# Optimization experiments

Measured on AMD Instinct MI355X. Metric: run time of the kernel, lower is better.

## Reference

```python
import jax, jax.numpy as jnp
import numpy as np

B, L, D, H = 32, 512, 512, 8          # batch(=num_nodes), seq len, model_size, num_heads
HD = D // H                            # head size
E_DIM, N_EDGES, N_PATHS = 128, 4096, 1024  # edge_dim (hardcoded 128), edge table, #(src,dst) pairs
MAXD = H                               # max_path_distance == num_heads


def setup_inputs() -> dict:
    rng = jax.random.key(0)
    ks = jax.random.split(rng, 16)
    n = lambda k, s: jax.random.normal(k, s, jnp.float32)
    idx = jnp.arange(N_PATHS)
    inp = {
        'query': n(ks[0], (B, L, D)),
        'key':   n(ks[1], (B, L, D)),
        'value': n(ks[2], (B, L, D)),
        'mask':  jnp.ones((B, 1, 1, L), jnp.float32),
        'edge_attr': n(ks[3], (N_EDGES, E_DIM)),
        'path_src': (idx // B).astype(jnp.int32),   # all (src,dst) node pairs
        'path_dst': (idx % B).astype(jnp.int32),
        'path_edges': jax.random.randint(ks[4], (N_PATHS, MAXD), 0, N_EDGES),
        'path_lens': jax.random.randint(ks[5], (N_PATHS,), 1, MAXD + 1),
        # learned params
        'WQ': n(ks[6], (D, D)) * 0.02, 'bQ': jnp.zeros((D,), jnp.float32),
        'WK': n(ks[7], (D, D)) * 0.02, 'bK': jnp.zeros((D,), jnp.float32),
        'WV': n(ks[8], (D, D)) * 0.02, 'bV': jnp.zeros((D,), jnp.float32),
        'WO': n(ks[9], (D, D)) * 0.02, 'bO': jnp.zeros((D,), jnp.float32),
        'edge_vector': n(ks[10], (MAXD, E_DIM)) * 0.05,  # EdgeEncoding weight
        'b_vec': n(ks[11], (MAXD,)) * 0.05,              # SpatialEncoding weight
        'b_scale': jnp.float32(0.001),
        'c_scale': jnp.float32(0.001),
    }
    return inp


def reference(query, key, value, mask, edge_attr, path_src, path_dst, path_edges,
              path_lens, WQ, bQ, WK, bK, WV, bV, WO, bO, edge_vector, b_vec,
              b_scale, c_scale):
    def split_heads(x):  # [B,L,D] -> [B,H,L,HD]
        return x.reshape(B, L, H, HD).transpose(0, 2, 1, 3)

    q = split_heads(jnp.einsum('bld,de->ble', query, WQ) + bQ)
    k = split_heads(jnp.einsum('bld,de->ble', key, WK) + bK)
    v = split_heads(jnp.einsum('bld,de->ble', value, WV) + bV)

    score = jnp.einsum('bhqd,bhkd->bhqk', q, k) / jnp.sqrt(jnp.float32(HD))

    pl = jnp.minimum(path_lens, MAXD).astype(jnp.int32)  # clipped path lengths

    # SpatialEncoding: spatial[src,dst] = b_vec[min(len,maxd)-1]
    spatial = jnp.zeros((B, B), jnp.float32).at[path_src, path_dst].set(b_vec[pl - 1])
    b_mean = spatial.mean(axis=1)  # [B]

    # EdgeEncoding: cij[src,dst] = mean_k <edge_vector[k], edge_attr[path[k]]>
    pe = edge_attr[path_edges]                       # [P,MAXD,E]  batched gather
    dots = jnp.einsum('ke,pke->pk', edge_vector, pe)  # [P,MAXD]
    kmask = (jnp.arange(MAXD)[None, :] < pl[:, None]).astype(jnp.float32)
    cvals = jnp.where(pl > 0, (dots * kmask).sum(1) / jnp.maximum(pl, 1), 0.0)
    cij = jnp.zeros((B, B), jnp.float32).at[path_src, path_dst].set(cvals)
    c_mean = cij.mean(axis=1)  # [B]

    bias = (b_scale * b_mean + c_scale * c_mean)[:, None, None, None]
    score = score + bias + (1.0 - mask) * (-1e9)

    alpha = jax.nn.softmax(score, axis=-1)
    ctx = jnp.einsum('bhqk,bhkd->bhqd', alpha, v)
    ctx = ctx.transpose(0, 2, 1, 3).reshape(B, L, D)
    return jnp.einsum('bld,de->ble', ctx, WO) + bO
```

## Files before the change

kernel.cpp:

```cpp
#include <hip/hip_runtime.h>
#include <hip/hip_bf16.h>

#define B_  32
#define L_  512
#define D_  512
#define H_  8
#define HD_ 64

typedef __attribute__((ext_vector_type(8))) short bf16x8;
typedef __attribute__((ext_vector_type(4))) short bf16x4;
typedef __attribute__((ext_vector_type(4))) float f32x4;

__device__ __forceinline__ short f2bf(float f) {
  union { float f; unsigned u; } x; x.f = f;
  unsigned r = x.u + 0x7FFFu + ((x.u >> 16) & 1u);
  return (short)(r >> 16);
}

__device__ __forceinline__ void gll16(const void* g, void* l) {
  __builtin_amdgcn_global_load_lds(
      (const __attribute__((address_space(1))) unsigned int*)g,
      (__attribute__((address_space(3))) unsigned int*)l, 16, 0, 0);
}

__device__ __forceinline__ bf16x8 cvt8(f32x4 a, f32x4 b) {
  union { __hip_bfloat162 h[4]; bf16x8 v; } u;
  u.h[0] = __float22bfloat162_rn(float2{a[0], a[1]});
  u.h[1] = __float22bfloat162_rn(float2{a[2], a[3]});
  u.h[2] = __float22bfloat162_rn(float2{b[0], b[1]});
  u.h[3] = __float22bfloat162_rn(float2{b[2], b[3]});
  return u.v;
}

#define DS_FENCE() do { asm volatile("s_waitcnt lgkmcnt(0)" ::: "memory"); \
                        __builtin_amdgcn_sched_barrier(0); } while (0)

__global__ __launch_bounds__(256) void wt_kernel(
    const float* __restrict__ WQ, const float* __restrict__ WK,
    const float* __restrict__ WV, const float* __restrict__ WO,
    short* __restrict__ wt) {
  __shared__ float tile[32][33];
  int wz = blockIdx.z;
  const float* W = (wz == 0) ? WQ : (wz == 1) ? WK : (wz == 2) ? WV : WO;
  int k0 = blockIdx.y * 32, n0 = blockIdx.x * 32;
  int tr = threadIdx.x >> 5, tc = threadIdx.x & 31;
#pragma unroll
  for (int i = 0; i < 4; ++i)
    tile[tr + i * 8][tc] = W[(size_t)(k0 + tr + i * 8) * D_ + n0 + tc];
  __syncthreads();
#pragma unroll
  for (int i = 0; i < 4; ++i)
    wt[((size_t)wz * D_ + n0 + tr + i * 8) * D_ + k0 + tc] =
        f2bf(tile[tc][tr + i * 8]);
}

__global__ __launch_bounds__(256, 3) void gemm_qkv(
    const float* __restrict__ Xq, const float* __restrict__ Xk,
    const float* __restrict__ Xv, const short* __restrict__ wt,
    const float* __restrict__ bQ, const float* __restrict__ bK,
    const float* __restrict__ bV,
    short* __restrict__ q_ws, short* __restrict__ k_ws,
    short* __restrict__ vt_ws) {
  __shared__ __align__(16) char lds[49152];

  int mode = blockIdx.z;
  const float* A = (mode == 0) ? Xq : (mode == 1) ? Xk : Xv;
  const short* WT = wt + (size_t)mode * D_ * D_;
  const float* bias = (mode == 0) ? bQ : (mode == 1) ? bK : bV;

  int wgid = blockIdx.x + 4 * blockIdx.y;
  int rr_ = wgid >> 3;
  int m0 = ((wgid & 7) * 16 + (rr_ >> 2)) * 128;
  int n0 = (rr_ & 3) * 128;

  int tid = threadIdx.x, lane = tid & 63, w = tid >> 6;
  int wr = w >> 1, wc = w & 1, g = lane >> 4, lr = lane & 15;

  int qa = lane >> 3, ca = (lane & 7) ^ qa;
  int qb = lane >> 2, cb = (lane & 3) ^ ((lane >> 3) & 3);

  auto stage = [&](int ks, int bs) {
    char* Ab = lds + bs * 16384;
    char* Bb = lds + 32768 + bs * 8192;
#pragma unroll
    for (int j = 0; j < 4; ++j) {
      int e = w * 4 + j, row = e * 8 + qa;
      gll16(A + (size_t)(m0 + row) * D_ + ks * 32 + ca * 4, Ab + e * 1024);
    }
#pragma unroll
    for (int j = 0; j < 2; ++j) {
      int e = w * 2 + j, row = e * 16 + qb;
      gll16(WT + (size_t)(n0 + row) * D_ + ks * 32 + cb * 8, Bb + e * 1024);
    }
  };

  stage(0, 0);
  __syncthreads();

  f32x4 acc[4][4] = {};
#pragma unroll
  for (int ks = 0; ks < 16; ++ks) {
    if (ks < 15) stage(ks + 1, (ks + 1) & 1);
    const char* Ab = lds + (ks & 1) * 16384;
    const char* Bb = lds + 32768 + (ks & 1) * 8192;
    bf16x8 af[4], bf_[4];
#pragma unroll
    for (int i = 0; i < 4; ++i) {
      int row = wr * 64 + i * 16 + lr;
      f32x4 lo = *(const f32x4*)(Ab + row * 128 + (((2 * g) ^ (lr & 7)) << 4));
      f32x4 hi = *(const f32x4*)(Ab + row * 128 + (((2 * g + 1) ^ (lr & 7)) << 4));
      af[i] = cvt8(lo, hi);
    }
#pragma unroll
    for (int i = 0; i < 4; ++i) {
      int row = wc * 64 + i * 16 + lr;
      bf_[i] = *(const bf16x8*)(Bb + row * 64 + ((g ^ ((lr >> 1) & 3)) << 4));
    }
#pragma unroll
    for (int mi = 0; mi < 4; ++mi)
#pragma unroll
      for (int nj = 0; nj < 4; ++nj)
        acc[mi][nj] = __builtin_amdgcn_mfma_f32_16x16x32_bf16(
            af[mi], bf_[nj], acc[mi][nj], 0, 0, 0);
    __syncthreads();
  }

#pragma unroll
  for (int mi = 0; mi < 4; ++mi) {
#pragma unroll
    for (int nj = 0; nj < 4; ++nj) {
      int n = n0 + wc * 64 + nj * 16 + lr;
      float bb = bias[n];
      int h = n >> 6, hd = n & 63;
#pragma unroll
      for (int rr = 0; rr < 4; ++rr) {
        int m = m0 + wr * 64 + mi * 16 + g * 4 + rr;
        int b = m >> 9, l = m & 511;
        short v = f2bf(acc[mi][nj][rr] + bb);
        if (mode == 0)
          q_ws[(((size_t)b * H_ + h) * L_ + l) * HD_ + hd] = v;
        else if (mode == 1)
          k_ws[(((size_t)b * H_ + h) * L_ + l) * HD_ + hd] = v;
        else
          vt_ws[(((size_t)b * H_ + h) * HD_ + hd) * L_ + l] = v;
      }
    }
  }
}

__global__ __launch_bounds__(256, 4) void attn_kernel(
    const short* __restrict__ q_ws, const short* __restrict__ k_ws,
    const short* __restrict__ vt_ws, const float* __restrict__ mask,
    short* __restrict__ ctx_ws) {
  __shared__ __align__(16) char lds[40960];
  int wg = blockIdx.x;
  int bh   = (wg & 7) * 32 + (wg >> 6);
  int qblk = (wg >> 3) & 7;
  int b = bh >> 3, h = bh & 7;
  int tid = threadIdx.x, lane = tid & 63, w = tid >> 6;
  int g = lane >> 4, lr = lane & 15;
  char* Pl = lds + 32768 + w * 2048;
  int qbase = qblk * 64 + w * 16;

  const short* Qh  = q_ws  + (size_t)bh * (L_ * HD_);
  const short* Kh  = k_ws  + (size_t)bh * (L_ * HD_);
  const short* VTh = vt_ws + (size_t)bh * (HD_ * L_);
  const float* mrow = mask + (size_t)b * L_;

  bf16x8 aq0 = *(const bf16x8*)(Qh + (size_t)(qbase + lr) * HD_ + g * 8);
  bf16x8 aq1 = *(const bf16x8*)(Qh + (size_t)(qbase + lr) * HD_ + 32 + g * 8);

  int rowin = lane >> 3;
  int sch8 = ((lane & 7) ^ rowin) * 8;

#pragma unroll
  for (int j = 0; j < 2; ++j) {
    int e = w * 2 + j, row = e * 8 + rowin;
    gll16(Kh + (size_t)row * HD_ + sch8, lds + e * 1024);
    gll16(VTh + (size_t)row * L_ + sch8, lds + 16384 + e * 1024);
  }
  __syncthreads();

  f32x4 c[4] = {};
  float m[4] = {-1e30f, -1e30f, -1e30f, -1e30f};
  float sum[4] = {0.f, 0.f, 0.f, 0.f};

  for (int ch = 0; ch < 8; ++ch) {
    const char* Kb = lds + (ch & 1) * 8192;
    const char* Vb = lds + 16384 + (ch & 1) * 8192;
    if (ch < 7) {
      char* Kn = lds + ((ch + 1) & 1) * 8192;
      char* Vn = lds + 16384 + ((ch + 1) & 1) * 8192;
#pragma unroll
      for (int j = 0; j < 2; ++j) {
        int e = w * 2 + j, row = e * 8 + rowin;
        gll16(Kh + ((size_t)(ch + 1) * 64 + row) * HD_ + sch8, Kn + e * 1024);
        gll16(VTh + (size_t)row * L_ + (ch + 1) * 64 + sch8, Vn + e * 1024);
      }
    }
    float mb[4];
#pragma unroll
    for (int kt = 0; kt < 4; ++kt)
      mb[kt] = (1.0f - mrow[ch * 64 + kt * 16 + lr]) * -1e9f;

    f32x4 s[4];
#pragma unroll
    for (int kt = 0; kt < 4; ++kt) {
      int row = kt * 16 + lr;
      bf16x8 bk0 = *(const bf16x8*)(Kb + row * 128 + ((g ^ (lr & 7)) << 4));
      bf16x8 bk1 = *(const bf16x8*)(Kb + row * 128 + (((4 + g) ^ (lr & 7)) << 4));
      f32x4 a = {0.f, 0.f, 0.f, 0.f};
      a = __builtin_amdgcn_mfma_f32_16x16x32_bf16(aq0, bk0, a, 0, 0, 0);
      a = __builtin_amdgcn_mfma_f32_16x16x32_bf16(aq1, bk1, a, 0, 0, 0);
#pragma unroll
      for (int rr = 0; rr < 4; ++rr) a[rr] = a[rr] * 0.125f + mb[kt];
      s[kt] = a;
    }

    float pmax[4], scl[4];
#pragma unroll
    for (int rr = 0; rr < 4; ++rr)
      pmax[rr] = fmaxf(fmaxf(s[0][rr], s[1][rr]), fmaxf(s[2][rr], s[3][rr]));
#pragma unroll
    for (int off = 1; off < 16; off <<= 1)
#pragma unroll
      for (int rr = 0; rr < 4; ++rr)
        pmax[rr] = fmaxf(pmax[rr], __shfl_xor(pmax[rr], off, 64));
#pragma unroll
    for (int rr = 0; rr < 4; ++rr) {
      float mn = fmaxf(m[rr], pmax[rr]);
      scl[rr] = __expf(m[rr] - mn);
      m[rr] = mn;
      sum[rr] *= scl[rr];
    }
#pragma unroll
    for (int nt = 0; nt < 4; ++nt)
#pragma unroll
      for (int rr = 0; rr < 4; ++rr) c[nt][rr] *= scl[rr];

#pragma unroll
    for (int kt = 0; kt < 4; ++kt) {
      int col2 = (kt * 16 + lr) * 2;
#pragma unroll
      for (int rr = 0; rr < 4; ++rr) {
        float p = __expf(s[kt][rr] - m[rr]);
        sum[rr] += p;
        int row = g * 4 + rr;
        *(short*)(Pl + row * 128 + (col2 ^ ((row & 7) << 4))) = f2bf(p);
      }
    }
    DS_FENCE();

#pragma unroll
    for (int kk = 0; kk < 2; ++kk) {
      bf16x8 ap = *(const bf16x8*)(Pl + lr * 128 +
                                   (((kk * 4 + g) ^ (lr & 7)) << 4));
#pragma unroll
      for (int nt = 0; nt < 4; ++nt) {
        int row = nt * 16 + lr;
        bf16x8 bv = *(const bf16x8*)(Vb + row * 128 +
                                     (((kk * 4 + g) ^ (lr & 7)) << 4));
        c[nt] = __builtin_amdgcn_mfma_f32_16x16x32_bf16(ap, bv, c[nt], 0, 0, 0);
      }
    }
    DS_FENCE();
    if (ch < 7) __syncthreads();
  }

  float inv[4];
#pragma unroll
  for (int off = 1; off < 16; off <<= 1)
#pragma unroll
    for (int rr = 0; rr < 4; ++rr) sum[rr] += __shfl_xor(sum[rr], off, 64);
#pragma unroll
  for (int rr = 0; rr < 4; ++rr) inv[rr] = 1.0f / sum[rr];

#pragma unroll
  for (int nt = 0; nt < 4; ++nt) {
    int hd = nt * 16 + lr;
#pragma unroll
    for (int rr = 0; rr < 4; ++rr) {
      int qrow = qbase + g * 4 + rr;
      ctx_ws[(((size_t)b * L_ + qrow) * H_ + h) * HD_ + hd] =
          f2bf(c[nt][rr] * inv[rr]);
    }
  }
}

__global__ __launch_bounds__(256, 3) void gemm_out(
    const short* __restrict__ ctx, const short* __restrict__ wt3,
    const float* __restrict__ bO, float* __restrict__ out) {
  __shared__ __align__(16) char lds[32768];
  int wgid = blockIdx.x + 4 * blockIdx.y;
  int rr_ = wgid >> 3;
  int m0 = ((wgid & 7) * 16 + (rr_ >> 2)) * 128;
  int n0 = (rr_ & 3) * 128;
  int tid = threadIdx.x, lane = tid & 63, w = tid >> 6;
  int wr = w >> 1, wc = w & 1, g = lane >> 4, lr = lane & 15;
  int qb = lane >> 2, cb = (lane & 3) ^ ((lane >> 3) & 3);

  auto stage = [&](int ks, int bs) {
    char* Ab = lds + bs * 8192;
    char* Bb = lds + 16384 + bs * 8192;
#pragma unroll
    for (int j = 0; j < 2; ++j) {
      int e = w * 2 + j, row = e * 16 + qb;
      gll16(ctx + (size_t)(m0 + row) * D_ + ks * 32 + cb * 8, Ab + e * 1024);
      gll16(wt3 + (size_t)(n0 + row) * D_ + ks * 32 + cb * 8, Bb + e * 1024);
    }
  };

  stage(0, 0);
  __syncthreads();

  f32x4 acc[4][4] = {};
#pragma unroll
  for (int ks = 0; ks < 16; ++ks) {
    if (ks < 15) stage(ks + 1, (ks + 1) & 1);
    const char* Ab = lds + (ks & 1) * 8192;
    const char* Bb = lds + 16384 + (ks & 1) * 8192;
    bf16x8 af[4], bf_[4];
#pragma unroll
    for (int i = 0; i < 4; ++i) {
      int row = wr * 64 + i * 16 + lr;
      af[i] = *(const bf16x8*)(Ab + row * 64 + ((g ^ ((lr >> 1) & 3)) << 4));
    }
#pragma unroll
    for (int i = 0; i < 4; ++i) {
      int row = wc * 64 + i * 16 + lr;
      bf_[i] = *(const bf16x8*)(Bb + row * 64 + ((g ^ ((lr >> 1) & 3)) << 4));
    }
#pragma unroll
    for (int mi = 0; mi < 4; ++mi)
#pragma unroll
      for (int nj = 0; nj < 4; ++nj)
        acc[mi][nj] = __builtin_amdgcn_mfma_f32_16x16x32_bf16(
            af[mi], bf_[nj], acc[mi][nj], 0, 0, 0);
    __syncthreads();
  }
#pragma unroll
  for (int mi = 0; mi < 4; ++mi) {
#pragma unroll
    for (int nj = 0; nj < 4; ++nj) {
      int n = n0 + wc * 64 + nj * 16 + lr;
      float bb = bO[n];
#pragma unroll
      for (int rr = 0; rr < 4; ++rr) {
        int m = m0 + wr * 64 + mi * 16 + g * 4 + rr;
        out[(size_t)m * D_ + n] = acc[mi][nj][rr] + bb;
      }
    }
  }
}

extern "C" void kernel_launch(void* const* d_in, const int* in_sizes, int n_in,
                              void* d_out, int out_size, void* d_ws,
                              size_t ws_size, hipStream_t stream) {
  const float* query = (const float*)d_in[0];
  const float* key   = (const float*)d_in[1];
  const float* value = (const float*)d_in[2];
  const float* mask  = (const float*)d_in[3];
  const float* WQ = (const float*)d_in[9];
  const float* bQ = (const float*)d_in[10];
  const float* WK = (const float*)d_in[11];
  const float* bK = (const float*)d_in[12];
  const float* WV = (const float*)d_in[13];
  const float* bV = (const float*)d_in[14];
  const float* WO = (const float*)d_in[15];
  const float* bO = (const float*)d_in[16];

  short* ws  = (short*)d_ws;
  short* wt  = ws;
  short* q   = ws + 1048576;
  short* k   = q + 8388608;
  short* vt  = k + 8388608;
  short* ctx = vt + 8388608;
  float* out = (float*)d_out;

  wt_kernel<<<dim3(16, 16, 4), 256, 0, stream>>>(WQ, WK, WV, WO, wt);
  gemm_qkv<<<dim3(4, 128, 3), 256, 0, stream>>>(query, key, value, wt,
                                                bQ, bK, bV, q, k, vt);
  attn_kernel<<<2048, 256, 0, stream>>>(q, k, vt, mask, ctx);
  gemm_out<<<dim3(4, 128), 256, 0, stream>>>(ctx, wt + 3 * 262144, bO, out);
}
```

Measured before the change: 133.0 us.

## Triple-buffer GEMM LDS staging with vmcnt waits and MFMA priority

```diff
diff --git a/kernel.cpp b/kernel.cpp
--- a/kernel.cpp
+++ b/kernel.cpp
@@ -34,6 +34,10 @@
 
 #define DS_FENCE() do { asm volatile("s_waitcnt lgkmcnt(0)" ::: "memory"); \
                         __builtin_amdgcn_sched_barrier(0); } while (0)
+#define VMCNT6 asm volatile("s_waitcnt vmcnt(6)" ::: "memory")
+#define VMCNT4 asm volatile("s_waitcnt vmcnt(4)" ::: "memory")
+#define VMCNT0 asm volatile("s_waitcnt vmcnt(0)" ::: "memory")
+#define SCHEDB __builtin_amdgcn_sched_barrier(0)
 
 __global__ __launch_bounds__(256) void wt_kernel(
     const float* __restrict__ WQ, const float* __restrict__ WK,
@@ -54,14 +58,14 @@
         f2bf(tile[tc][tr + i * 8]);
 }
 
-__global__ __launch_bounds__(256, 3) void gemm_qkv(
+__global__ __launch_bounds__(256, 2) void gemm_qkv(
     const float* __restrict__ Xq, const float* __restrict__ Xk,
     const float* __restrict__ Xv, const short* __restrict__ wt,
     const float* __restrict__ bQ, const float* __restrict__ bK,
     const float* __restrict__ bV,
     short* __restrict__ q_ws, short* __restrict__ k_ws,
     short* __restrict__ vt_ws) {
-  __shared__ __align__(16) char lds[49152];
+  __shared__ __align__(16) char lds[73728];
 
   int mode = blockIdx.z;
   const float* A = (mode == 0) ? Xq : (mode == 1) ? Xk : Xv;
@@ -76,33 +80,42 @@
   int tid = threadIdx.x, lane = tid & 63, w = tid >> 6;
   int wr = w >> 1, wc = w & 1, g = lane >> 4, lr = lane & 15;
 
-  int qa = lane >> 3, ca = (lane & 7) ^ qa;
-  int qb = lane >> 2, cb = (lane & 3) ^ ((lane >> 3) & 3);
-
-  auto stage = [&](int ks, int bs) {
-    char* Ab = lds + bs * 16384;
-    char* Bb = lds + 32768 + bs * 8192;
+  int ca = (lane & 7) ^ (lane >> 3);
+  int cb = (lane & 3) ^ ((lane >> 2) & 3);
+
+  auto stageA = [&](int ks, int bi) {
+    char* Ab = lds + bi * 16384;
 #pragma unroll
     for (int j = 0; j < 4; ++j) {
-      int e = w * 4 + j, row = e * 8 + qa;
+      int e = w * 4 + j, row = e * 8 + (lane >> 3);
       gll16(A + (size_t)(m0 + row) * D_ + ks * 32 + ca * 4, Ab + e * 1024);
     }
+  };
+  auto stageB = [&](int ks, int bi) {
+    char* Bb = lds + 49152 + bi * 8192;
 #pragma unroll
     for (int j = 0; j < 2; ++j) {
-      int e = w * 2 + j, row = e * 16 + qb;
+      int e = w * 2 + j, row = e * 16 + (lane >> 2);
       gll16(WT + (size_t)(n0 + row) * D_ + ks * 32 + cb * 8, Bb + e * 1024);
     }
   };
 
-  stage(0, 0);
-  __syncthreads();
+  stageA(0, 0); stageB(0, 0);
+  stageA(1, 1); stageB(1, 1);
+  VMCNT6;
+  __builtin_amdgcn_s_barrier();
+  SCHEDB;
 
   f32x4 acc[4][4] = {};
 #pragma unroll
-  for (int ks = 0; ks < 16; ++ks) {
-    if (ks < 15) stage(ks + 1, (ks + 1) & 1);
-    const char* Ab = lds + (ks & 1) * 16384;
-    const char* Bb = lds + 32768 + (ks & 1) * 8192;
+  for (int t = 0; t < 16; ++t) {
+    if (t < 14) {
+      stageA(t + 2, (t + 2) % 3);
+      stageB(t + 2, (t + 2) % 3);
+      SCHEDB;
+    }
+    const char* Ab = lds + (t % 3) * 16384;
+    const char* Bb = lds + 49152 + (t % 3) * 8192;
     bf16x8 af[4], bf_[4];
 #pragma unroll
     for (int i = 0; i < 4; ++i) {
@@ -114,15 +127,22 @@
 #pragma unroll
     for (int i = 0; i < 4; ++i) {
       int row = wc * 64 + i * 16 + lr;
-      bf_[i] = *(const bf16x8*)(Bb + row * 64 + ((g ^ ((lr >> 1) & 3)) << 4));
-    }
+      bf_[i] = *(const bf16x8*)(Bb + row * 64 + ((g ^ (lr & 3)) << 4));
+    }
+    __builtin_amdgcn_s_setprio(1);
 #pragma unroll
     for (int mi = 0; mi < 4; ++mi)
 #pragma unroll
       for (int nj = 0; nj < 4; ++nj)
         acc[mi][nj] = __builtin_amdgcn_mfma_f32_16x16x32_bf16(
             af[mi], bf_[nj], acc[mi][nj], 0, 0, 0);
-    __syncthreads();
+    __builtin_amdgcn_s_setprio(0);
+    if (t < 15) {
+      if (t < 14) { VMCNT6; }
+      else       { VMCNT0; }
+      __builtin_amdgcn_s_barrier();
+      SCHEDB;
+    }
   }
 
 #pragma unroll
@@ -290,53 +310,73 @@
 __global__ __launch_bounds__(256, 3) void gemm_out(
     const short* __restrict__ ctx, const short* __restrict__ wt3,
     const float* __restrict__ bO, float* __restrict__ out) {
-  __shared__ __align__(16) char lds[32768];
+  __shared__ __align__(16) char lds[49152];
   int wgid = blockIdx.x + 4 * blockIdx.y;
   int rr_ = wgid >> 3;
   int m0 = ((wgid & 7) * 16 + (rr_ >> 2)) * 128;
   int n0 = (rr_ & 3) * 128;
   int tid = threadIdx.x, lane = tid & 63, w = tid >> 6;
   int wr = w >> 1, wc = w & 1, g = lane >> 4, lr = lane & 15;
-  int qb = lane >> 2, cb = (lane & 3) ^ ((lane >> 3) & 3);
-
-  auto stage = [&](int ks, int bs) {
-    char* Ab = lds + bs * 8192;
-    char* Bb = lds + 16384 + bs * 8192;
+  int cb = (lane & 3) ^ ((lane >> 2) & 3);
+
+  auto stageA = [&](int ks, int bi) {
+    char* Ab = lds + bi * 8192;
 #pragma unroll
     for (int j = 0; j < 2; ++j) {
-      int e = w * 2 + j, row = e * 16 + qb;
+      int e = w * 2 + j, row = e * 16 + (lane >> 2);
       gll16(ctx + (size_t)(m0 + row) * D_ + ks * 32 + cb * 8, Ab + e * 1024);
+    }
+  };
+  auto stageB = [&](int ks, int bi) {
+    char* Bb = lds + 24576 + bi * 8192;
+#pragma unroll
+    for (int j = 0; j < 2; ++j) {
+      int e = w * 2 + j, row = e * 16 + (lane >> 2);
       gll16(wt3 + (size_t)(n0 + row) * D_ + ks * 32 + cb * 8, Bb + e * 1024);
     }
   };
 
-  stage(0, 0);
-  __syncthreads();
+  stageA(0, 0); stageB(0, 0);
+  stageA(1, 1); stageB(1, 1);
+  VMCNT4;
+  __builtin_amdgcn_s_barrier();
+  SCHEDB;
 
   f32x4 acc[4][4] = {};
 #pragma unroll
-  for (int ks = 0; ks < 16; ++ks) {
-    if (ks < 15) stage(ks + 1, (ks + 1) & 1);
-    const char* Ab = lds + (ks & 1) * 8192;
-    const char* Bb = lds + 16384 + (ks & 1) * 8192;
+  for (int t = 0; t < 16; ++t) {
+    if (t < 14) {
+      stageA(t + 2, (t + 2) % 3);
+      stageB(t + 2, (t + 2) % 3);
+      SCHEDB;
+    }
+    const char* Ab = lds + (t % 3) * 8192;
+    const char* Bb = lds + 24576 + (t % 3) * 8192;
     bf16x8 af[4], bf_[4];
 #pragma unroll
     for (int i = 0; i < 4; ++i) {
       int row = wr * 64 + i * 16 + lr;
-      af[i] = *(const bf16x8*)(Ab + row * 64 + ((g ^ ((lr >> 1) & 3)) << 4));
+      af[i] = *(const bf16x8*)(Ab + row * 64 + ((g ^ (lr & 3)) << 4));
     }
 #pragma unroll
     for (int i = 0; i < 4; ++i) {
       int row = wc * 64 + i * 16 + lr;
-      bf_[i] = *(const bf16x8*)(Bb + row * 64 + ((g ^ ((lr >> 1) & 3)) << 4));
-    }
+      bf_[i] = *(const bf16x8*)(Bb + row * 64 + ((g ^ (lr & 3)) << 4));
+    }
+    __builtin_amdgcn_s_setprio(1);
 #pragma unroll
     for (int mi = 0; mi < 4; ++mi)
 #pragma unroll
       for (int nj = 0; nj < 4; ++nj)
         acc[mi][nj] = __builtin_amdgcn_mfma_f32_16x16x32_bf16(
             af[mi], bf_[nj], acc[mi][nj], 0, 0, 0);
-    __syncthreads();
+    __builtin_amdgcn_s_setprio(0);
+    if (t < 15) {
+      if (t < 14) { VMCNT4; }
+      else       { VMCNT0; }
+      __builtin_amdgcn_s_barrier();
+      SCHEDB;
+    }
   }
 #pragma unroll
   for (int mi = 0; mi < 4; ++mi) {
```

After: 129.9 us. 1.02x faster.
